# Kernel tuning notes

Hardware: AMD Instinct MI355X
Metric: run time of the kernel (lower is better)

The kernel has to match this reference:

```python
import jax, jax.numpy as jnp
import numpy as np

SXY_BF, SC_BF = 70.0, 12.0
COMPAT_BF, COMPAT_SPATIAL = 4.0, 2.0
SXY_SPATIAL = 6
NUM_ITER = 5
N_OUT = 21


def _gkern_depthwise(std, chans):
    # matches gkern(): sig_sq even -> r = sig_sq - 1, s = 2r+1
    sig_sq = std ** 2
    r = sig_sq if sig_sq % 2 else sig_sq - 1
    s = 2 * r + 1
    yy, xx = np.meshgrid(np.arange(s), np.arange(s), indexing='ij')
    k = np.exp(-(((yy - r) ** 2 + (xx - r) ** 2) / (2.0 * sig_sq)))
    k = k / k.sum()
    # original builds a [C,C,s,s] diagonal kernel == depthwise [C,1,s,s]
    return jnp.asarray(np.broadcast_to(k[None, None], (chans, 1, s, s)).copy(), jnp.float32)


def setup_inputs() -> dict:
    key = jax.random.key(0)
    k1, k2 = jax.random.split(key)
    unary = jax.random.uniform(k1, (2, N_OUT, 64, 64), dtype=jnp.float32)
    ref = jax.random.uniform(k2, (2, 3, 64, 64), dtype=jnp.float32) * 255.0  # RGB image
    gk = _gkern_depthwise(SXY_SPATIAL, N_OUT)
    kstd = jnp.asarray([SXY_BF, SXY_BF, SC_BF, SC_BF, SC_BF], jnp.float32)
    return {"unary": unary, "ref": ref, "gk": gk, "kstd": kstd}


def _crf_forward(unary, ref, gk, kstd):
    N, C, H, W = unary.shape
    P = H * W
    # stacked reference features: [y, x, r, g, b]
    yy, xx = jnp.meshgrid(jnp.arange(H, dtype=jnp.float32),
                          jnp.arange(W, dtype=jnp.float32), indexing='ij')
    grid = jnp.broadcast_to(jnp.stack([yy, xx])[None], (N, 2, H, W))
    stacked = jnp.concatenate([grid, ref], axis=1)  # [N,5,H,W]
    feats = (stacked / kstd[None, :, None, None]).reshape(N, -1, P).transpose(0, 2, 1)  # [N,P,5]
    # exact dense Gaussian (bilateral) kernel: K[p,q] = exp(-||f_p - f_q||^2 / 2)
    sq = jnp.sum(feats * feats, axis=-1)  # [N,P]
    d2 = sq[:, :, None] + sq[:, None, :] - 2.0 * jnp.einsum('npd,nqd->npq', feats, feats)
    K = jnp.exp(-0.5 * jnp.maximum(d2, 0.0))  # [N,P,P]

    U = jnp.log(jnp.clip(unary, 1e-5, 1.0))
    q = jax.nn.softmax(U, axis=1)
    pad = gk.shape[-1] // 2
    for i in range(NUM_ITER):
        qbf = jnp.einsum('npq,ncq->ncp', K, q.reshape(N, C, P)).reshape(N, C, H, W)
        qsf = jax.lax.conv_general_dilated(
            q, gk, window_strides=(1, 1), padding=[(pad, pad), (pad, pad)],
            feature_group_count=C, dimension_numbers=('NCHW', 'OIHW', 'NCHW'))
        q_hat = U + COMPAT_BF * qbf + COMPAT_SPATIAL * qsf
        q = jax.nn.softmax(q_hat, axis=1)  # normalize_final_iter=True
    return q


def reference(unary, ref, gk, kstd):
    return _crf_forward(unary, ref, gk, kstd)
```

## Files before the change

kernel.cpp:

```cpp
#include <hip/hip_runtime.h>
#include <math.h>

#ifndef __has_builtin
#define __has_builtin(x) 0
#endif
#if __has_builtin(__builtin_amdgcn_exp2f)
#define EXP2F(x) __builtin_amdgcn_exp2f(x)
#else
#define EXP2F(x) exp2f(x)
#endif

#define L2E  1.44269504088896340736f
#define RL2E 0.69314718055994530942f

#define NBATCH 2
#define NC 21
#define HH 64
#define WW 64
#define NP 4096
#define KR 35
#define KS 71

typedef _Float16 half_t;
typedef _Float16 h8 __attribute__((ext_vector_type(8)));
typedef _Float16 h4 __attribute__((ext_vector_type(4)));
typedef float f4 __attribute__((ext_vector_type(4)));
#define MFMA16(a, b, c) __builtin_amdgcn_mfma_f32_16x16x32_f16((a), (b), (c), 0, 0, 0)

#define PTILE 256
#define NPT   16
#define SQ    16
#define CHUNK 256
#define NBBIL (NBATCH * NPT * SQ)
#define NBCONV (NBATCH * NC)
#define SEGS_PER_S 1024
#define SEG_HALVES 256

#define OFF_QFEAT 0
#define OFF_UT    65536
#define OFF_QSF   262144
#define OFF_G     434176
#define OFF_QH16  436224
#define OFF_QBFC  534528
#define OFF_PART  796672

#define LDS_BYTES 27648

__global__ __launch_bounds__(256) void setup_kernel(
    const float* __restrict__ unary, const float* __restrict__ ref,
    const float* __restrict__ kstd, float* __restrict__ ws,
    float* __restrict__ outq)
{
    int gid = blockIdx.x * 256 + threadIdx.x;
    if (gid < 4096) {
        float s = 0.f;
        for (int t = -KR; t <= KR; ++t) s += expf(-(float)(t * t) * (1.0f / 72.0f));
        int y = gid >> 6, yp = gid & 63;
        int d = y - yp;
        float v = (d >= -KR && d <= KR) ? expf(-(float)(d * d) * (1.0f / 72.0f)) / s : 0.f;
        ((half_t*)(ws + OFF_G))[gid] = (half_t)v;
    }
    if (gid >= NBATCH * NP) return;
    int n = gid >> 12, p = gid & (NP - 1);
    int y = p >> 6, x = p & 63;
    float k0 = kstd[0], k1 = kstd[1], k2 = kstd[2], k3 = kstd[3], k4 = kstd[4];
    const float* rp = ref + n * 3 * NP + p;
    float f0 = (float)y / k0;
    float f1 = (float)x / k1;
    float f2 = rp[0]      / k2;
    float f3 = rp[NP]     / k3;
    float f4 = rp[2 * NP] / k4;
    float sq = f0*f0 + f1*f1 + f2*f2 + f3*f3 + f4*f4;
    float h  = -0.5f * L2E * sq;
    float* qf = ws + OFF_QFEAT + gid * 8;
    qf[0]=L2E*f0; qf[1]=L2E*f1; qf[2]=L2E*f2; qf[3]=L2E*f3; qf[4]=L2E*f4;
    qf[5]=h; qf[6]=0.f; qf[7]=0.f;

    float U[NC], e[NC];
    const float* up = unary + n * NC * NP + p;
    float m = -1e30f;
    for (int c = 0; c < NC; ++c) {
        float u = up[c * NP];
        u = fminf(fmaxf(u, 1e-5f), 1.0f);
        U[c] = logf(u);
        m = fmaxf(m, U[c]);
    }
    float ssum = 0.f;
    for (int c = 0; c < NC; ++c) { e[c] = EXP2F(L2E * (U[c] - m)); ssum += e[c]; }
    float inv = 1.0f / ssum;
    float* ut = ws + OFF_UT + gid * 24;
    half_t* qh = (half_t*)(ws + OFF_QH16);
    for (int c = 0; c < NC; ++c) {
        float qv = e[c] * inv;
        ut[c] = U[c];
        qh[(n * 24 + c) * NP + p] = (half_t)qv;
        outq[(n * NC + c) * NP + p] = qv;
    }
    ut[21] = 0.f; ut[22] = 0.f; ut[23] = 0.f;
    qh[(n * 24 + 21) * NP + p] = (half_t)0.f;
    qh[(n * 24 + 22) * NP + p] = (half_t)0.f;
    qh[(n * 24 + 23) * NP + p] = (half_t)0.f;
}

__global__ __launch_bounds__(256) void bilat_conv_kernel(
    const float* __restrict__ qfeat,
    const half_t* __restrict__ qh16,
    const half_t* __restrict__ gmat,
    half_t* __restrict__ part,
    float* __restrict__ qsf)
{
    __shared__ __align__(16) char lds[LDS_BYTES];
    int b = blockIdx.x;
    int tid = threadIdx.x;
    int l = tid & 63, w = tid >> 6;

    if (b < NBBIL) {
        int n  = b & 1;
        int pt = (b >> 1) & (NPT - 1);
        int s  = b >> 5;
        float*  qfeatS = (float*)lds;
        half_t* qls    = (half_t*)(lds + 8192);

        {
            const float4* src = (const float4*)(qfeat + (size_t)(n * NP + s * CHUNK) * 8);
            float4* dst = (float4*)qfeatS;
            for (int i = tid; i < CHUNK * 2; i += 256) dst[i] = src[i];
        }
        {
            for (int i = tid; i < 21 * (CHUNK / 8); i += 256) {
                int c = i >> 5, g = i & 31;
                *(h8*)(qls + c * 264 + g * 8) =
                    *(const h8*)(qh16 + (size_t)(n * 24 + c) * NP + s * CHUNK + g * 8);
            }
            for (int i = tid; i < 11 * 33; i += 256) {
                int c = 21 + i / 33, g = i % 33;
                *(h8*)(qls + c * 264 + g * 8) = (h8)(half_t)0.f;
            }
        }
        float pf[4][5], ph[4];
        #pragma unroll
        for (int mt = 0; mt < 4; ++mt) {
            const float* fp = qfeat + (size_t)(n * NP + pt * PTILE + (w * 4 + mt) * 16 + (l & 15)) * 8;
            #pragma unroll
            for (int i = 0; i < 5; ++i) pf[mt][i] = fp[i] * RL2E;
            ph[mt] = fp[5];
        }
        f4 acc[4][2];
        #pragma unroll
        for (int mt = 0; mt < 4; ++mt) {
            acc[mt][0] = (f4)0.f; acc[mt][1] = (f4)0.f;
        }
        int kq = (l >> 4) * 8;
        __syncthreads();

        for (int step = 0; step < CHUNK / 32; ++step) {
            h8 kv[4];
            #pragma unroll
            for (int j = 0; j < 8; ++j) {
                int ql = step * 32 + kq + j;
                float4 qa = *(const float4*)(qfeatS + ql * 8);
                float2 qb = *(const float2*)(qfeatS + ql * 8 + 4);
                #pragma unroll
                for (int mt = 0; mt < 4; ++mt) {
                    float e = ph[mt] + qb.y;
                    e = fmaf(pf[mt][0], qa.x, e);
                    e = fmaf(pf[mt][1], qa.y, e);
                    e = fmaf(pf[mt][2], qa.z, e);
                    e = fmaf(pf[mt][3], qa.w, e);
                    e = fmaf(pf[mt][4], qb.x, e);
                    kv[mt][j] = (half_t)EXP2F(e);
                }
            }
            h8 bf0 = *(const h8*)(qls + (size_t)(l & 15) * 264 + step * 32 + kq);
            h8 bf1 = *(const h8*)(qls + (size_t)(16 + (l & 15)) * 264 + step * 32 + kq);
            #pragma unroll
            for (int mt = 0; mt < 4; ++mt) {
                acc[mt][0] = MFMA16(kv[mt], bf0, acc[mt][0]);
                acc[mt][1] = MFMA16(kv[mt], bf1, acc[mt][1]);
            }
        }
        #pragma unroll
        for (int mt = 0; mt < 4; ++mt) {
            #pragma unroll
            for (int cht = 0; cht < 2; ++cht) {
                int segFlat = ((((s * 2 + n) * NPT + pt) * 4 + w) * 4 + mt) * 2 + cht;
                h4 hv;
                hv[0] = (half_t)acc[mt][cht][0];
                hv[1] = (half_t)acc[mt][cht][1];
                hv[2] = (half_t)acc[mt][cht][2];
                hv[3] = (half_t)acc[mt][cht][3];
                *(h4*)(part + (size_t)segFlat * SEG_HALVES + l * 4) = hv;
            }
        }
    } else {
        int cb = b - NBBIL;
        int n = cb / NC, c = cb % NC;
        half_t* qt = (half_t*)lds;
        half_t* gl = (half_t*)(lds + 9216);
        half_t* dl = (half_t*)(lds + 18432);

        for (int i = tid; i < 512; i += 256) {
            int row = i >> 3, g = i & 7;
            *(h8*)(gl + row * 72 + g * 8) = *(const h8*)(gmat + row * 64 + g * 8);
        }
        const half_t* qsrc = qh16 + (size_t)(n * 24 + c) * NP;
        for (int i = tid; i < 512; i += 256) {
            int row = i >> 3, g = i & 7;
            h8 v = *(const h8*)(qsrc + row * 64 + g * 8);
            #pragma unroll
            for (int k = 0; k < 8; ++k) qt[(g * 8 + k) * 72 + row] = v[k];
        }
        __syncthreads();

        int m0 = w * 16;
        f4 acc1[4];
        #pragma unroll
        for (int nt = 0; nt < 4; ++nt) acc1[nt] = (f4)0.f;
        #pragma unroll
        for (int ks = 0; ks < 2; ++ks) {
            h8 af = *(const h8*)(gl + (size_t)(m0 + (l & 15)) * 72 + ks * 32 + (l >> 4) * 8);
            #pragma unroll
            for (int nt = 0; nt < 4; ++nt) {
                h8 bf = *(const h8*)(qt + (size_t)(nt * 16 + (l & 15)) * 72 + ks * 32 + (l >> 4) * 8);
                acc1[nt] = MFMA16(af, bf, acc1[nt]);
            }
        }
        #pragma unroll
        for (int nt = 0; nt < 4; ++nt)
            #pragma unroll
            for (int r = 0; r < 4; ++r)
                dl[(size_t)(m0 + (l >> 4) * 4 + r) * 72 + nt * 16 + (l & 15)] = (half_t)acc1[nt][r];
        __syncthreads();

        f4 acc2[4];
        #pragma unroll
        for (int nt = 0; nt < 4; ++nt) acc2[nt] = (f4)0.f;
        #pragma unroll
        for (int ks = 0; ks < 2; ++ks) {
            h8 af = *(const h8*)(dl + (size_t)(m0 + (l & 15)) * 72 + ks * 32 + (l >> 4) * 8);
            #pragma unroll
            for (int nt = 0; nt < 4; ++nt) {
                h8 bf = *(const h8*)(gl + (size_t)(nt * 16 + (l & 15)) * 72 + ks * 32 + (l >> 4) * 8);
                acc2[nt] = MFMA16(af, bf, acc2[nt]);
            }
        }
        float* dst = qsf + (size_t)(n * NC + c) * NP;
        #pragma unroll
        for (int nt = 0; nt < 4; ++nt)
            #pragma unroll
            for (int r = 0; r < 4; ++r)
                dst[(size_t)(m0 + (l >> 4) * 4 + r) * 64 + nt * 16 + (l & 15)] = acc2[nt][r];
    }
}

__global__ __launch_bounds__(256) void reduce_kernel(
    const half_t* __restrict__ part, float* __restrict__ qbfC)
{
    int tIdx = blockIdx.x * 256 + threadIdx.x;
    int segLocal = tIdx >> 6, lane = tIdx & 63;
    float a0 = 0.f, a1 = 0.f, a2 = 0.f, a3 = 0.f;
    for (int s = 0; s < SQ; ++s) {
        h4 v = *(const h4*)(part + ((size_t)(s * SEGS_PER_S + segLocal)) * SEG_HALVES + lane * 4);
        a0 += (float)v[0]; a1 += (float)v[1]; a2 += (float)v[2]; a3 += (float)v[3];
    }
    *(float4*)(qbfC + (size_t)segLocal * SEG_HALVES + lane * 4) = make_float4(a0, a1, a2, a3);
}

__global__ __launch_bounds__(256) void update_kernel(
    const float* __restrict__ qbfC, const float* __restrict__ ut_,
    const float* __restrict__ qsf, float* __restrict__ outq,
    half_t* __restrict__ qh16)
{
    int gid = blockIdx.x * 256 + threadIdx.x;
    int n = gid >> 12, p = gid & (NP - 1);
    int pt = p >> 8, pp = p & 255;
    int mt = pp >> 4, mrow = pp & 15;
    int wv = mt >> 2, mtl = mt & 3;
    int lg = mrow >> 2, reg = mrow & 3;
    int segBase = (((n * NPT + pt) * 4 + wv) * 4 + mtl) * 2;

    float qb[NC];
    #pragma unroll
    for (int c = 0; c < NC; ++c) {
        int cht = c >> 4, chL = c & 15;
        qb[c] = qbfC[(size_t)(segBase + cht) * SEG_HALVES + (lg * 16 + chL) * 4 + reg];
    }
    const float* ut = ut_ + (size_t)gid * 24;
    const float* qs = qsf + (size_t)n * NC * NP + p;
    float lg_[NC], e[NC];
    float m = -1e30f;
    #pragma unroll
    for (int c = 0; c < NC; ++c) {
        float li = ut[c] + 4.0f * qb[c] + 2.0f * qs[c * NP];
        lg_[c] = li;
        m = fmaxf(m, li);
    }
    float ssum = 0.f;
    #pragma unroll
    for (int c = 0; c < NC; ++c) { e[c] = EXP2F(L2E * (lg_[c] - m)); ssum += e[c]; }
    float inv = 1.0f / ssum;
    #pragma unroll
    for (int c = 0; c < NC; ++c) {
        float qv = e[c] * inv;
        outq[(size_t)(n * NC + c) * NP + p] = qv;
        qh16[(size_t)(n * 24 + c) * NP + p] = (half_t)qv;
    }
}

extern "C" void kernel_launch(void* const* d_in, const int* in_sizes, int n_in,
                              void* d_out, int out_size, void* d_ws, size_t ws_size,
                              hipStream_t stream)
{
    const float* unary = (const float*)d_in[0];
    const float* ref   = (const float*)d_in[1];
    const float* kstd  = (const float*)d_in[3];
    float* ws   = (float*)d_ws;
    float* outq = (float*)d_out;

    const float*  qfeat = ws + OFF_QFEAT;
    float*        ut    = ws + OFF_UT;
    float*        qsf   = ws + OFF_QSF;
    const half_t* gmat  = (const half_t*)(ws + OFF_G);
    half_t*       qh16  = (half_t*)(ws + OFF_QH16);
    float*        qbfC  = ws + OFF_QBFC;
    half_t*       part  = (half_t*)(ws + OFF_PART);

    setup_kernel<<<32, 256, 0, stream>>>(unary, ref, kstd, ws, outq);
    for (int it = 0; it < 5; ++it) {
        bilat_conv_kernel<<<NBBIL + NBCONV, 256, 0, stream>>>(qfeat, qh16, gmat, part, qsf);
        reduce_kernel<<<256, 256, 0, stream>>>(part, qbfC);
        update_kernel<<<32, 256, 0, stream>>>(qbfC, ut, qsf, outq, qh16);
    }
}
```

Baseline: 179.5 us.

## Double split-K blocks for bilateral pass and store features SoA in LDS

The bilateral kernel now splits the key dimension into 32 chunks of 128 instead of 16 chunks of 256, which doubles the number of work blocks. The aim is better occupancy and load balance across CUs. Setup also writes a structure-of-arrays copy of the scaled features, which the kernel stages into LDS as scalar per-dimension reads, with a padded q row stride, to cut LDS bank conflicts. In exchange, the reduce kernel must sum twice as many fp16 partials, and the extra global traffic and rounding may offset the gain.

```diff
diff --git a/kernel.cpp b/kernel.cpp
--- a/kernel.cpp
+++ b/kernel.cpp
@@ -15,8 +15,6 @@
 
 #define NBATCH 2
 #define NC 21
-#define HH 64
-#define WW 64
 #define NP 4096
 #define KR 35
 #define KS 71
@@ -29,22 +27,25 @@
 
 #define PTILE 256
 #define NPT   16
-#define SQ    16
-#define CHUNK 256
+#define SQ    32
+#define CHUNK 128
+#define STEPS 4
 #define NBBIL (NBATCH * NPT * SQ)
 #define NBCONV (NBATCH * NC)
 #define SEGS_PER_S 1024
 #define SEG_HALVES 256
 
 #define OFF_QFEAT 0
-#define OFF_UT    65536
-#define OFF_QSF   262144
-#define OFF_G     434176
-#define OFF_QH16  436224
-#define OFF_QBFC  534528
-#define OFF_PART  796672
+#define OFF_QSOA  65536
+#define OFF_UT    114688
+#define OFF_QSF   311296
+#define OFF_G     483328
+#define OFF_QH16  485376
+#define OFF_QBFC  583680
+#define OFF_PART  845824
 
 #define LDS_BYTES 27648
+#define QLS_STRIDE 272
 
 __global__ __launch_bounds__(256) void setup_kernel(
     const float* __restrict__ unary, const float* __restrict__ ref,
@@ -67,14 +68,18 @@
     const float* rp = ref + n * 3 * NP + p;
     float f0 = (float)y / k0;
     float f1 = (float)x / k1;
-    float f2 = rp[0]      / k2;
+    float f2_ = rp[0]      / k2;
     float f3 = rp[NP]     / k3;
-    float f4 = rp[2 * NP] / k4;
-    float sq = f0*f0 + f1*f1 + f2*f2 + f3*f3 + f4*f4;
+    float f4_ = rp[2 * NP] / k4;
+    float sq = f0*f0 + f1*f1 + f2_*f2_ + f3*f3 + f4_*f4_;
     float h  = -0.5f * L2E * sq;
     float* qf = ws + OFF_QFEAT + gid * 8;
-    qf[0]=L2E*f0; qf[1]=L2E*f1; qf[2]=L2E*f2; qf[3]=L2E*f3; qf[4]=L2E*f4;
+    qf[0]=L2E*f0; qf[1]=L2E*f1; qf[2]=L2E*f2_; qf[3]=L2E*f3; qf[4]=L2E*f4_;
     qf[5]=h; qf[6]=0.f; qf[7]=0.f;
+    float* qs = ws + OFF_QSOA;
+    qs[0*8192 + gid] = L2E*f0;  qs[1*8192 + gid] = L2E*f1;
+    qs[2*8192 + gid] = L2E*f2_; qs[3*8192 + gid] = L2E*f3;
+    qs[4*8192 + gid] = L2E*f4_; qs[5*8192 + gid] = h;
 
     float U[NC], e[NC];
     const float* up = unary + n * NC * NP + p;
@@ -103,7 +108,8 @@
 }
 
 __global__ __launch_bounds__(256) void bilat_conv_kernel(
-    const float* __restrict__ qfeat,
+    const float* __restrict__ qfeatA,
+    const float* __restrict__ qsoa,
     const half_t* __restrict__ qh16,
     const half_t* __restrict__ gmat,
     half_t* __restrict__ part,
@@ -118,61 +124,62 @@
         int n  = b & 1;
         int pt = (b >> 1) & (NPT - 1);
         int s  = b >> 5;
-        float*  qfeatS = (float*)lds;
-        half_t* qls    = (half_t*)(lds + 8192);
-
-        {
-            const float4* src = (const float4*)(qfeat + (size_t)(n * NP + s * CHUNK) * 8);
-            float4* dst = (float4*)qfeatS;
-            for (int i = tid; i < CHUNK * 2; i += 256) dst[i] = src[i];
-        }
-        {
-            for (int i = tid; i < 21 * (CHUNK / 8); i += 256) {
-                int c = i >> 5, g = i & 31;
-                *(h8*)(qls + c * 264 + g * 8) =
-                    *(const h8*)(qh16 + (size_t)(n * 24 + c) * NP + s * CHUNK + g * 8);
-            }
-            for (int i = tid; i < 11 * 33; i += 256) {
-                int c = 21 + i / 33, g = i % 33;
-                *(h8*)(qls + c * 264 + g * 8) = (h8)(half_t)0.f;
-            }
+        float*  qsoaS = (float*)lds;
+        half_t* qls   = (half_t*)(lds + 3072);
+
+        for (int i = tid; i < 6 * (CHUNK / 4); i += 256) {
+            int d = i >> 5, g = i & 31;
+            *(f4*)(qsoaS + d * CHUNK + g * 4) =
+                *(const f4*)(qsoa + (size_t)d * 8192 + n * NP + s * CHUNK + g * 4);
+        }
+        for (int i = tid; i < 21 * (CHUNK / 8); i += 256) {
+            int c = i >> 4, g = i & 15;
+            *(h8*)(qls + c * QLS_STRIDE + g * 8) =
+                *(const h8*)(qh16 + (size_t)(n * 24 + c) * NP + s * CHUNK + g * 8);
+        }
+        for (int i = tid; i < 11 * (CHUNK / 8); i += 256) {
+            int c = 21 + (i >> 4), g = i & 15;
+            *(h8*)(qls + c * QLS_STRIDE + g * 8) = (h8)(half_t)0.f;
         }
         float pf[4][5], ph[4];
         #pragma unroll
         for (int mt = 0; mt < 4; ++mt) {
-            const float* fp = qfeat + (size_t)(n * NP + pt * PTILE + (w * 4 + mt) * 16 + (l & 15)) * 8;
+            const float* fp = qfeatA + (size_t)(n * NP + pt * PTILE + (w * 4 + mt) * 16 + (l & 15)) * 8;
             #pragma unroll
             for (int i = 0; i < 5; ++i) pf[mt][i] = fp[i] * RL2E;
             ph[mt] = fp[5];
         }
         f4 acc[4][2];
         #pragma unroll
-        for (int mt = 0; mt < 4; ++mt) {
-            acc[mt][0] = (f4)0.f; acc[mt][1] = (f4)0.f;
-        }
+        for (int mt = 0; mt < 4; ++mt) { acc[mt][0] = (f4)0.f; acc[mt][1] = (f4)0.f; }
         int kq = (l >> 4) * 8;
         __syncthreads();
 
-        for (int step = 0; step < CHUNK / 32; ++step) {
+        for (int step = 0; step < STEPS; ++step) {
+            int qbase = step * 32 + kq;
             h8 kv[4];
             #pragma unroll
             for (int j = 0; j < 8; ++j) {
-                int ql = step * 32 + kq + j;
-                float4 qa = *(const float4*)(qfeatS + ql * 8);
-                float2 qb = *(const float2*)(qfeatS + ql * 8 + 4);
+                int ql = qbase + j;
+                float q0 = qsoaS[0 * CHUNK + ql];
+                float q1 = qsoaS[1 * CHUNK + ql];
+                float q2 = qsoaS[2 * CHUNK + ql];
+                float q3 = qsoaS[3 * CHUNK + ql];
+                float q4 = qsoaS[4 * CHUNK + ql];
+                float qh = qsoaS[5 * CHUNK + ql];
                 #pragma unroll
                 for (int mt = 0; mt < 4; ++mt) {
-                    float e = ph[mt] + qb.y;
-                    e = fmaf(pf[mt][0], qa.x, e);
-                    e = fmaf(pf[mt][1], qa.y, e);
-                    e = fmaf(pf[mt][2], qa.z, e);
-                    e = fmaf(pf[mt][3], qa.w, e);
-                    e = fmaf(pf[mt][4], qb.x, e);
+                    float e = ph[mt] + qh;
+                    e = fmaf(pf[mt][0], q0, e);
+                    e = fmaf(pf[mt][1], q1, e);
+                    e = fmaf(pf[mt][2], q2, e);
+                    e = fmaf(pf[mt][3], q3, e);
+                    e = fmaf(pf[mt][4], q4, e);
                     kv[mt][j] = (half_t)EXP2F(e);
                 }
             }
-            h8 bf0 = *(const h8*)(qls + (size_t)(l & 15) * 264 + step * 32 + kq);
-            h8 bf1 = *(const h8*)(qls + (size_t)(16 + (l & 15)) * 264 + step * 32 + kq);
+            h8 bf0 = *(const h8*)(qls + (size_t)(l & 15) * QLS_STRIDE + qbase);
+            h8 bf1 = *(const h8*)(qls + (size_t)(16 + (l & 15)) * QLS_STRIDE + qbase);
             #pragma unroll
             for (int mt = 0; mt < 4; ++mt) {
                 acc[mt][0] = MFMA16(kv[mt], bf0, acc[mt][0]);
@@ -317,17 +324,19 @@
     float* ws   = (float*)d_ws;
     float* outq = (float*)d_out;
 
-    const float*  qfeat = ws + OFF_QFEAT;
-    float*        ut    = ws + OFF_UT;
-    float*        qsf   = ws + OFF_QSF;
-    const half_t* gmat  = (const half_t*)(ws + OFF_G);
-    half_t*       qh16  = (half_t*)(ws + OFF_QH16);
-    float*        qbfC  = ws + OFF_QBFC;
-    half_t*       part  = (half_t*)(ws + OFF_PART);
+    const float*  qfeatA = ws + OFF_QFEAT;
+    const float*  qsoa   = ws + OFF_QSOA;
+    float*        ut     = ws + OFF_UT;
+    float*        qsf    = ws + OFF_QSF;
+    const half_t* gmat   = (const half_t*)(ws + OFF_G);
+    half_t*       qh16   = (half_t*)(ws + OFF_QH16);
+    float*        qbfC   = ws + OFF_QBFC;
+    half_t*       part   = (half_t*)(ws + OFF_PART);
 
     setup_kernel<<<32, 256, 0, stream>>>(unary, ref, kstd, ws, outq);
     for (int it = 0; it < 5; ++it) {
-        bilat_conv_kernel<<<NBBIL + NBCONV, 256, 0, stream>>>(qfeat, qh16, gmat, part, qsf);
+        bilat_conv_kernel<<<NBBIL + NBCONV, 256, 0, stream>>>(
+            qfeatA, qsoa, qh16, gmat, part, qsf);
         reduce_kernel<<<256, 256, 0, stream>>>(part, qbfC);
         update_kernel<<<32, 256, 0, stream>>>(qbfC, ut, qsf, outq, qh16);
     }
```

Measured after the change: 198.4 us. 10.5% more time.
